# Optimization experiments

Measured on AMD Instinct MI355X. Metric: run time of the kernel, lower is better.

Reference implementation:

```python
import jax, jax.numpy as jnp
import numpy as np

TOPK = 10
NC = 80
ALPHA = 1.0
BETA = 6.0
EPS = 1e-8
IOU_EPS = 1e-7


def setup_inputs() -> dict:
    key = jax.random.key(0)
    ks = jax.random.split(key, 7)
    B, M, C = 32, 40, NC
    img = 640
    pts = []
    for s in (8, 16, 32):
        n = img // s
        xs = (jnp.arange(n, dtype=jnp.float32) + 0.5) * s
        gy, gx = jnp.meshgrid(xs, xs, indexing="ij")
        pts.append(jnp.stack([gx.ravel(), gy.ravel()], axis=-1))
    anchor_points = jnp.concatenate(pts, axis=0)  # (8400, 2)
    A = anchor_points.shape[0]
    pred_scores = jax.random.uniform(ks[0], (B, A, C), dtype=jnp.float32)
    ctr = anchor_points[None] + jax.random.normal(ks[1], (B, A, 2), dtype=jnp.float32) * 8.0
    wh = jax.random.uniform(ks[2], (B, A, 2), minval=16.0, maxval=128.0, dtype=jnp.float32)
    pred_boxes = jnp.concatenate([ctr - wh / 2, ctr + wh / 2], axis=-1)
    gctr = jax.random.uniform(ks[3], (B, M, 2), minval=64.0, maxval=576.0, dtype=jnp.float32)
    gwh = jax.random.uniform(ks[4], (B, M, 2), minval=32.0, maxval=256.0, dtype=jnp.float32)
    gt_boxes = jnp.concatenate([gctr - gwh / 2, gctr + gwh / 2], axis=-1)
    gt_labels = jax.random.randint(ks[5], (B, M, 1), 0, C)
    gt_mask = jax.random.uniform(ks[6], (B, M, 1)) < 0.8
    return {
        "pred_scores": pred_scores,
        "pred_boxes": pred_boxes,
        "anchor_points": anchor_points,
        "gt_labels": gt_labels,
        "gt_boxes": gt_boxes,
        "gt_mask": gt_mask,
    }


def reference(pred_scores, pred_boxes, anchor_points, gt_labels, gt_boxes, gt_mask):
    B, A, C = pred_scores.shape
    M = gt_boxes.shape[1]
    dt = pred_scores.dtype
    gtm = gt_mask[..., 0].astype(dt)  # (B, M)
    cls = gt_labels[..., 0].astype(jnp.int32)  # (B, M)
    b_idx = jnp.arange(B)[:, None]

    # --- step 1: anchor centers inside GT boxes ---
    lt = gt_boxes[:, :, None, :2]  # (B, M, 1, 2)
    rb = gt_boxes[:, :, None, 2:]
    ap = anchor_points[None, None, :, :]  # (1, 1, A, 2)
    deltas = jnp.concatenate([ap - lt, rb - ap], axis=-1)  # (B, M, A, 4)
    in_gt = (jnp.min(deltas, axis=-1) > EPS).astype(dt)  # (B, M, A)
    valid = in_gt * gtm[:, :, None]

    # --- alignment metric: cls score gathered per GT label, IoU(gt, pred) ---
    scores = pred_scores[b_idx, :, cls] * valid  # (B, M, A)
    gt = gt_boxes[:, :, None, :]  # (B, M, 1, 4)
    pd = pred_boxes[:, None, :, :]  # (B, 1, A, 4)
    iw = jnp.clip(jnp.minimum(gt[..., 2], pd[..., 2]) - jnp.maximum(gt[..., 0], pd[..., 0]), 0.0)
    ih = jnp.clip(jnp.minimum(gt[..., 3], pd[..., 3]) - jnp.maximum(gt[..., 1], pd[..., 1]), 0.0)
    inter = iw * ih
    area_g = (gt[..., 2] - gt[..., 0]) * (gt[..., 3] - gt[..., 1])
    area_p = (pd[..., 2] - pd[..., 0]) * (pd[..., 3] - pd[..., 1])
    ious = jnp.clip(inter / (area_g + area_p - inter + IOU_EPS), 0.0) * valid  # (B, M, A)
    align = (scores ** ALPHA) * (ious ** BETA)

    # --- step 2: top-k candidates per GT with duplicate suppression ---
    _, topk_idxs = jax.lax.top_k(align, TOPK)  # (B, M, K)
    km = jnp.broadcast_to(gt_mask[..., 0][:, :, None], topk_idxs.shape)
    topk_idxs = jnp.where(km, topk_idxs, 0)
    counts = jnp.zeros((B, M, A), dtype=jnp.int32)
    counts = counts.at[b_idx[:, :, None], jnp.arange(M)[None, :, None], topk_idxs].add(1)
    counts = jnp.where(counts > 1, 0, counts)
    mask = counts.astype(dt) * in_gt * gtm[:, :, None]  # (B, M, A)

    # --- step 4: resolve anchors assigned to multiple GTs by highest IoU ---
    fg = mask.sum(axis=1)  # (B, A)
    max_iou_onehot = jax.nn.one_hot(jnp.argmax(ious, axis=1), M, axis=1, dtype=dt)
    mask = jnp.where(fg[:, None, :] > 1, max_iou_onehot, mask)
    fg = mask.sum(axis=1)
    tgt_idx = jnp.argmax(mask, axis=1)  # (B, A)

    # --- targets ---
    target_labels = jnp.clip(jnp.take_along_axis(cls, tgt_idx, axis=1), 0, NC)  # (B, A)
    target_boxes = jnp.take_along_axis(gt_boxes, tgt_idx[..., None], axis=1)  # (B, A, 4)
    target_scores = jax.nn.one_hot(target_labels, NC, dtype=dt)
    target_scores = jnp.where(fg[..., None] > 0, target_scores, 0.0)

    # --- normalize scores by aligned metric ---
    align = align * mask
    pos_align = jnp.max(align, axis=-1, keepdims=True)  # (B, M, 1)
    pos_iou = jnp.max(ious * mask, axis=-1, keepdims=True)
    norm = jnp.max(align * pos_iou / (pos_align + EPS), axis=-2)[..., None]  # (B, A, 1)
    target_scores = target_scores * norm
    return target_labels, target_boxes, target_scores, fg > 0
```

## Files before the change

kernel.cpp:

```cpp
#include <hip/hip_runtime.h>
#include <cstdint>

#define TOPK_K 10
#define NCLS   80
#define EPS_F     1e-8f
#define IOU_EPS_F 1e-7f

__global__ void k_prep(const unsigned char* __restrict__ gm, int n,
                       int* __restrict__ gmask)
{
    __shared__ int anynz;
    if (threadIdx.x == 0) anynz = 0;
    __syncthreads();
    for (int i = threadIdx.x; i < n; i += blockDim.x) {
        if ((i & 3) && gm[i]) anynz = 1;
    }
    __syncthreads();
    const int is_int32 = (anynz == 0);
    const int* gi = (const int*)gm;
    for (int i = threadIdx.x; i < n; i += blockDim.x) {
        gmask[i] = is_int32 ? (gi[i] != 0) : (gm[i] != 0);
    }
}

__global__ __launch_bounds__(256) void k_topk(
    const float*  __restrict__ ps,
    const float4* __restrict__ pb,
    const float2* __restrict__ apts,
    const int*    __restrict__ gl,
    const float4* __restrict__ gb,
    const int*    __restrict__ gmask,
    unsigned long long* __restrict__ mask_bits,
    int B, int A, int C, int M)
{
    const int bm = blockIdx.x;
    if (!gmask[bm]) return;
    const int b = bm / M;
    const int m = bm - b * M;

    const float4 g = gb[bm];
    const float gx0 = g.x, gy0 = g.y, gx1 = g.z, gy1 = g.w;
    const float areag = (gx1 - gx0) * (gy1 - gy0);
    const int cls = gl[bm];
    const float*  psb = ps + (size_t)b * A * C + cls;
    const float4* pbb = pb + (size_t)b * A;

    float tv[TOPK_K]; int ti[TOPK_K];
#pragma unroll
    for (int i = 0; i < TOPK_K; ++i) { tv[i] = -1.0f; ti[i] = 0x7fffffff; }

    for (int a = threadIdx.x; a < A; a += blockDim.x) {
        const float2 an = apts[a];
        const float d = fminf(fminf(an.x - gx0, an.y - gy0),
                              fminf(gx1 - an.x, gy1 - an.y));
        float al = 0.0f;
        if (d > EPS_F) {
            const float4 p = pbb[a];
            const float iw = fmaxf(fminf(gx1, p.z) - fmaxf(gx0, p.x), 0.0f);
            const float ih = fmaxf(fminf(gy1, p.w) - fmaxf(gy0, p.y), 0.0f);
            const float inter = iw * ih;
            const float areap = (p.z - p.x) * (p.w - p.y);
            const float iou = fmaxf(inter / (areag + areap - inter + IOU_EPS_F), 0.0f);
            const float sc = psb[(size_t)a * C];
            const float i2 = iou * iou;
            al = sc * (i2 * i2 * i2);
        }
        if ((al > tv[TOPK_K - 1]) ||
            (al == tv[TOPK_K - 1] && a < ti[TOPK_K - 1])) {
            float cv = al; int ci = a;
#pragma unroll
            for (int q = 0; q < TOPK_K; ++q) {
                const bool bet = (cv > tv[q]) || (cv == tv[q] && ci < ti[q]);
                if (bet) {
                    const float tv_ = tv[q]; const int ti_ = ti[q];
                    tv[q] = cv; ti[q] = ci; cv = tv_; ci = ti_;
                }
            }
        }
    }

    __shared__ float sv[256];
    __shared__ int   si[256];
    const unsigned long long bit = 1ull << m;
    int p = 0;
    for (int r = 0; r < TOPK_K; ++r) {
        sv[threadIdx.x] = (p < TOPK_K) ? tv[p] : -1.0f;
        si[threadIdx.x] = (p < TOPK_K) ? ti[p] : 0x7fffffff;
        const int myci = si[threadIdx.x];
        __syncthreads();
        for (int s = 128; s > 0; s >>= 1) {
            if (threadIdx.x < s) {
                const float ov = sv[threadIdx.x + s];
                const int   oi = si[threadIdx.x + s];
                if ((ov > sv[threadIdx.x]) ||
                    (ov == sv[threadIdx.x] && oi < si[threadIdx.x])) {
                    sv[threadIdx.x] = ov; si[threadIdx.x] = oi;
                }
            }
            __syncthreads();
        }
        const int widx = si[0];
        if (threadIdx.x == 0 && widx != 0x7fffffff) {
            const float2 an = apts[widx];
            const float d = fminf(fminf(an.x - gx0, an.y - gy0),
                                  fminf(gx1 - an.x, gy1 - an.y));
            if (d > EPS_F)
                atomicOr(&mask_bits[(size_t)b * A + widx], bit);
        }
        if (myci == widx) ++p;
        __syncthreads();
    }
}

__global__ __launch_bounds__(256) void k_resolve(
    const float*  __restrict__ ps,
    const float4* __restrict__ pb,
    const float2* __restrict__ apts,
    const int*    __restrict__ gl,
    const float4* __restrict__ gb,
    const int*    __restrict__ gmask,
    const unsigned long long* __restrict__ mask_bits,
    int*          __restrict__ assign,
    float*        __restrict__ aval,
    unsigned int* __restrict__ pos_align,
    unsigned int* __restrict__ pos_iou,
    float*        __restrict__ out,
    int B, int A, int C, int M)
{
    const int id = blockIdx.x * blockDim.x + threadIdx.x;
    if (id >= B * A) return;
    const int b = id / A;
    const int a = id - b * A;

    const unsigned long long bits = mask_bits[id];
    const int cnt = __popcll(bits);
    int t = 0, fg = 0;
    const float2 an = apts[a];
    const float4 p  = pb[id];
    const float areap = (p.z - p.x) * (p.w - p.y);

    if (cnt == 1) {
        t = __ffsll(bits) - 1; fg = 1;
    } else if (cnt > 1) {
        float best = -1.0f; int bi = 0;
        for (int mm = 0; mm < M; ++mm) {
            const float4 gg = gb[b * M + mm];
            const float d = fminf(fminf(an.x - gg.x, an.y - gg.y),
                                  fminf(gg.z - an.x, gg.w - an.y));
            float iou = 0.0f;
            if (d > EPS_F && gmask[b * M + mm]) {
                const float iw = fmaxf(fminf(gg.z, p.z) - fmaxf(gg.x, p.x), 0.0f);
                const float ih = fmaxf(fminf(gg.w, p.w) - fmaxf(gg.y, p.y), 0.0f);
                const float inter = iw * ih;
                const float areag = (gg.z - gg.x) * (gg.w - gg.y);
                iou = fmaxf(inter / (areag + areap - inter + IOU_EPS_F), 0.0f);
            }
            if (iou > best) { best = iou; bi = mm; }
        }
        t = bi; fg = 1;
    }

    float av = 0.0f;
    if (fg) {
        const float4 gg = gb[b * M + t];
        const float d = fminf(fminf(an.x - gg.x, an.y - gg.y),
                              fminf(gg.z - an.x, gg.w - an.y));
        if (d > EPS_F && gmask[b * M + t]) {
            const float iw = fmaxf(fminf(gg.z, p.z) - fmaxf(gg.x, p.x), 0.0f);
            const float ih = fmaxf(fminf(gg.w, p.w) - fmaxf(gg.y, p.y), 0.0f);
            const float inter = iw * ih;
            const float areag = (gg.z - gg.x) * (gg.w - gg.y);
            const float iou = fmaxf(inter / (areag + areap - inter + IOU_EPS_F), 0.0f);
            const float sc = ps[((size_t)b * A + a) * C + gl[b * M + t]];
            const float i2 = iou * iou;
            av = sc * (i2 * i2 * i2);
            atomicMax(&pos_align[b * M + t], __float_as_uint(av));
            atomicMax(&pos_iou[b * M + t],  __float_as_uint(iou));
        }
    }

    assign[id] = t;
    aval[id]   = av;

    int lab = gl[b * M + t];
    lab = lab < 0 ? 0 : (lab > NCLS ? NCLS : lab);
    out[id] = (float)lab;
    ((float4*)(out + (size_t)B * A))[id] = gb[b * M + t];
    out[(size_t)B * A * (5 + C) + id] = fg ? 1.0f : 0.0f;
}

__global__ void k_norm(const int* __restrict__ assign,
                       const float* __restrict__ aval,
                       const unsigned int* __restrict__ pos_align,
                       const unsigned int* __restrict__ pos_iou,
                       float* __restrict__ normv, int BA, int A, int M)
{
    const int id = blockIdx.x * blockDim.x + threadIdx.x;
    if (id >= BA) return;
    const int b = id / A;
    const int t = assign[id];
    const float pa = __uint_as_float(pos_align[b * M + t]);
    const float pi = __uint_as_float(pos_iou[b * M + t]);
    normv[id] = aval[id] * pi / (pa + EPS_F);
}

__global__ void k_scores(const float* __restrict__ labels,
                         const float* __restrict__ normv,
                         float4* __restrict__ scores, int BA, int C4)
{
    const int gid = blockIdx.x * blockDim.x + threadIdx.x;
    if (gid >= BA * C4) return;
    const int row = gid / C4;
    const int c4  = gid - row * C4;
    const int lab = (int)labels[row];
    const float nv = normv[row];
    const int cb = c4 * 4;
    float4 v;
    v.x = (cb + 0 == lab) ? nv : 0.0f;
    v.y = (cb + 1 == lab) ? nv : 0.0f;
    v.z = (cb + 2 == lab) ? nv : 0.0f;
    v.w = (cb + 3 == lab) ? nv : 0.0f;
    scores[gid] = v;
}

extern "C" void kernel_launch(void* const* d_in, const int* in_sizes, int n_in,
                              void* d_out, int out_size, void* d_ws, size_t ws_size,
                              hipStream_t stream)
{
    const float*  ps = (const float*)d_in[0];
    const float4* pb = (const float4*)d_in[1];
    const float2* ap = (const float2*)d_in[2];
    const int*    gl = (const int*)d_in[3];
    const float4* gb = (const float4*)d_in[4];
    const unsigned char* gm = (const unsigned char*)d_in[5];

    const int A = in_sizes[2] / 2;
    const int B = in_sizes[1] / (A * 4);
    const int M = in_sizes[4] / (B * 4);
    const int C = in_sizes[0] / (B * A);
    const int BA = B * A;

    size_t off = 0;
    auto alloc = [&](size_t bytes) {
        void* p = (char*)d_ws + off;
        off += (bytes + 255) & ~(size_t)255;
        return p;
    };
    unsigned long long* mask_bits = (unsigned long long*)alloc((size_t)BA * 8);
    unsigned int* pos_a = (unsigned int*)alloc((size_t)B * M * 4);
    unsigned int* pos_i = (unsigned int*)alloc((size_t)B * M * 4);
    const size_t zero_bytes = off;
    int*   gmask  = (int*)alloc((size_t)B * M * 4);
    int*   assign = (int*)alloc((size_t)BA * 4);
    float* aval   = (float*)alloc((size_t)BA * 4);
    float* normv  = (float*)alloc((size_t)BA * 4);

    hipMemsetAsync(d_ws, 0, zero_bytes, stream);

    k_prep<<<1, 256, 0, stream>>>(gm, B * M, gmask);

    k_topk<<<B * M, 256, 0, stream>>>(ps, pb, ap, gl, gb, gmask, mask_bits,
                                      B, A, C, M);

    float* out = (float*)d_out;
    k_resolve<<<(BA + 255) / 256, 256, 0, stream>>>(
        ps, pb, ap, gl, gb, gmask, mask_bits,
        assign, aval, pos_a, pos_i, out, B, A, C, M);

    k_norm<<<(BA + 255) / 256, 256, 0, stream>>>(assign, aval, pos_a, pos_i,
                                                 normv, BA, A, M);

    const int C4 = C / 4;
    const int tot = BA * C4;
    k_scores<<<(tot + 255) / 256, 256, 0, stream>>>(
        out, normv, (float4*)(out + (size_t)BA * 5), BA, C4);
}
```

Baseline: 234.7 us.

## Precompute alignment matrix via coalesced score tiles, then top-k over dense rows

Adds a k_align kernel that loads 64-anchor tiles of the full score rows into shared memory with coalesced float4 reads. It computes the alignment metric for all GTs of a batch and stores it as a dense (B,M,A) buffer. This replaces the strided per-GT gathers of one class column in the old top-k kernel. Top-k now scans contiguous float4 rows using packed 64-bit keys and a wavefront shuffle reduction instead of a shared-memory tree. The memset and norm kernels are folded into the prep and score kernels, and a fallback path is kept for when the workspace is too small to hold the extra buffer.

```diff
diff --git a/kernel.cpp b/kernel.cpp
--- a/kernel.cpp
+++ b/kernel.cpp
@@ -5,9 +5,14 @@
 #define NCLS   80
 #define EPS_F     1e-8f
 #define IOU_EPS_F 1e-7f
+#define CH 64
+
+typedef unsigned long long u64;
 
 __global__ void k_prep(const unsigned char* __restrict__ gm, int n,
-                       int* __restrict__ gmask)
+                       int* __restrict__ gmask,
+                       unsigned int* __restrict__ pos_a,
+                       unsigned int* __restrict__ pos_i)
 {
     __shared__ int anynz;
     if (threadIdx.x == 0) anynz = 0;
@@ -20,106 +25,167 @@
     const int* gi = (const int*)gm;
     for (int i = threadIdx.x; i < n; i += blockDim.x) {
         gmask[i] = is_int32 ? (gi[i] != 0) : (gm[i] != 0);
-    }
-}
-
-__global__ __launch_bounds__(256) void k_topk(
+        pos_a[i] = 0u;
+        pos_i[i] = 0u;
+    }
+}
+
+__global__ __launch_bounds__(256) void k_align(
     const float*  __restrict__ ps,
     const float4* __restrict__ pb,
     const float2* __restrict__ apts,
     const int*    __restrict__ gl,
     const float4* __restrict__ gb,
     const int*    __restrict__ gmask,
-    unsigned long long* __restrict__ mask_bits,
-    int B, int A, int C, int M)
+    float*        __restrict__ align,
+    u64*          __restrict__ mask_bits,
+    int B, int A, int C, int M, int NCH)
+{
+    const int blk = blockIdx.x;
+    const int b  = blk / NCH;
+    const int ch = blk - b * NCH;
+    const int a0 = ch * CH;
+    const int aN = min(CH, A - a0);
+    const int tid = threadIdx.x;
+
+    __shared__ float  ssc[CH][81];
+    __shared__ float4 sgb[64];
+    __shared__ int    scls[64];
+    __shared__ int    sgm[64];
+
+    if (tid < aN) mask_bits[(size_t)b * A + a0 + tid] = 0ull;
+    if (tid < M) {
+        sgb[tid]  = gb[b * M + tid];
+        scls[tid] = gl[b * M + tid];
+        sgm[tid]  = gmask[b * M + tid];
+    }
+
+    const int C4 = C >> 2;
+    const float4* psrow = (const float4*)(ps + ((size_t)b * A + a0) * C);
+    for (int idx = tid; idx < aN * C4; idx += 256) {
+        const int r  = idx / C4;
+        const int c4 = idx - r * C4;
+        const float4 v = psrow[(size_t)r * C4 + c4];
+        float* dst = &ssc[r][c4 * 4];
+        dst[0] = v.x; dst[1] = v.y; dst[2] = v.z; dst[3] = v.w;
+    }
+    __syncthreads();
+
+    const int asub = tid & (CH - 1);
+    const int m0   = tid >> 6;
+    const bool act = (asub < aN);
+    float2 an = make_float2(0.f, 0.f);
+    float4 p  = make_float4(0.f, 0.f, 0.f, 0.f);
+    float areap = 0.f;
+    if (act) {
+        an = apts[a0 + asub];
+        p  = pb[(size_t)b * A + a0 + asub];
+        areap = (p.z - p.x) * (p.w - p.y);
+    }
+    for (int m = m0; m < M; m += 4) {
+        if (!act) continue;
+        float al = 0.f;
+        if (sgm[m]) {
+            const float4 g = sgb[m];
+            const float d = fminf(fminf(an.x - g.x, an.y - g.y),
+                                  fminf(g.z - an.x, g.w - an.y));
+            if (d > EPS_F) {
+                const float iw = fmaxf(fminf(g.z, p.z) - fmaxf(g.x, p.x), 0.f);
+                const float ih = fmaxf(fminf(g.w, p.w) - fmaxf(g.y, p.y), 0.f);
+                const float inter = iw * ih;
+                const float areag = (g.z - g.x) * (g.w - g.y);
+                const float iou = fmaxf(inter / (areag + areap - inter + IOU_EPS_F), 0.f);
+                const float sc = ssc[asub][scls[m]];
+                const float i2 = iou * iou;
+                al = sc * (i2 * i2 * i2);
+            }
+        }
+        align[((size_t)b * M + m) * A + a0 + asub] = al;
+    }
+}
+
+#define INS10(val, idx)                                                     \
+    {                                                                       \
+        u64 key = ((u64)__float_as_uint(val) << 32) |                       \
+                  (unsigned)(~(unsigned)(idx));                             \
+        if (key > kk[9]) {                                                  \
+            _Pragma("unroll")                                               \
+            for (int q = 0; q < 10; ++q) {                                  \
+                if (key > kk[q]) { u64 t_ = kk[q]; kk[q] = key; key = t_; } \
+            }                                                               \
+        }                                                                   \
+    }
+
+__global__ __launch_bounds__(256) void k_topk2(
+    const float4* __restrict__ align4,
+    const float2* __restrict__ apts,
+    const int*    __restrict__ gmask,
+    const float4* __restrict__ gb,
+    u64*          __restrict__ mask_bits,
+    int B, int A, int M)
 {
     const int bm = blockIdx.x;
     if (!gmask[bm]) return;
     const int b = bm / M;
     const int m = bm - b * M;
+    const int tid = threadIdx.x;
 
     const float4 g = gb[bm];
-    const float gx0 = g.x, gy0 = g.y, gx1 = g.z, gy1 = g.w;
-    const float areag = (gx1 - gx0) * (gy1 - gy0);
-    const int cls = gl[bm];
-    const float*  psb = ps + (size_t)b * A * C + cls;
-    const float4* pbb = pb + (size_t)b * A;
-
-    float tv[TOPK_K]; int ti[TOPK_K];
-#pragma unroll
-    for (int i = 0; i < TOPK_K; ++i) { tv[i] = -1.0f; ti[i] = 0x7fffffff; }
-
-    for (int a = threadIdx.x; a < A; a += blockDim.x) {
-        const float2 an = apts[a];
-        const float d = fminf(fminf(an.x - gx0, an.y - gy0),
-                              fminf(gx1 - an.x, gy1 - an.y));
-        float al = 0.0f;
-        if (d > EPS_F) {
-            const float4 p = pbb[a];
-            const float iw = fmaxf(fminf(gx1, p.z) - fmaxf(gx0, p.x), 0.0f);
-            const float ih = fmaxf(fminf(gy1, p.w) - fmaxf(gy0, p.y), 0.0f);
-            const float inter = iw * ih;
-            const float areap = (p.z - p.x) * (p.w - p.y);
-            const float iou = fmaxf(inter / (areag + areap - inter + IOU_EPS_F), 0.0f);
-            const float sc = psb[(size_t)a * C];
-            const float i2 = iou * iou;
-            al = sc * (i2 * i2 * i2);
-        }
-        if ((al > tv[TOPK_K - 1]) ||
-            (al == tv[TOPK_K - 1] && a < ti[TOPK_K - 1])) {
-            float cv = al; int ci = a;
-#pragma unroll
-            for (int q = 0; q < TOPK_K; ++q) {
-                const bool bet = (cv > tv[q]) || (cv == tv[q] && ci < ti[q]);
-                if (bet) {
-                    const float tv_ = tv[q]; const int ti_ = ti[q];
-                    tv[q] = cv; ti[q] = ci; cv = tv_; ci = ti_;
-                }
-            }
-        }
-    }
-
-    __shared__ float sv[256];
-    __shared__ int   si[256];
-    const unsigned long long bit = 1ull << m;
-    int p = 0;
+    const float4* row = align4 + (size_t)bm * (A >> 2);
+    const int n4 = A >> 2;
+
+    u64 kk[10];
+#pragma unroll
+    for (int q = 0; q < 10; ++q) kk[q] = 0ull;
+
+    for (int i = tid; i < n4; i += 256) {
+        const float4 v = row[i];
+        const int a4 = i * 4;
+        INS10(v.x, a4 + 0);
+        INS10(v.y, a4 + 1);
+        INS10(v.z, a4 + 2);
+        INS10(v.w, a4 + 3);
+    }
+
+    __shared__ u64 swv[4];
+    const u64 bit = 1ull << m;
     for (int r = 0; r < TOPK_K; ++r) {
-        sv[threadIdx.x] = (p < TOPK_K) ? tv[p] : -1.0f;
-        si[threadIdx.x] = (p < TOPK_K) ? ti[p] : 0x7fffffff;
-        const int myci = si[threadIdx.x];
+        u64 cur = kk[0];
+#pragma unroll
+        for (int off = 32; off; off >>= 1) {
+            const u64 o = __shfl_xor(cur, off);
+            cur = (o > cur) ? o : cur;
+        }
+        if ((tid & 63) == 0) swv[tid >> 6] = cur;
         __syncthreads();
-        for (int s = 128; s > 0; s >>= 1) {
-            if (threadIdx.x < s) {
-                const float ov = sv[threadIdx.x + s];
-                const int   oi = si[threadIdx.x + s];
-                if ((ov > sv[threadIdx.x]) ||
-                    (ov == sv[threadIdx.x] && oi < si[threadIdx.x])) {
-                    sv[threadIdx.x] = ov; si[threadIdx.x] = oi;
-                }
-            }
-            __syncthreads();
-        }
-        const int widx = si[0];
-        if (threadIdx.x == 0 && widx != 0x7fffffff) {
-            const float2 an = apts[widx];
-            const float d = fminf(fminf(an.x - gx0, an.y - gy0),
-                                  fminf(gx1 - an.x, gy1 - an.y));
+        const u64 w01 = (swv[0] > swv[1]) ? swv[0] : swv[1];
+        const u64 w23 = (swv[2] > swv[3]) ? swv[2] : swv[3];
+        const u64 win = (w01 > w23) ? w01 : w23;
+        if (kk[0] == win) {
+#pragma unroll
+            for (int q = 0; q < 9; ++q) kk[q] = kk[q + 1];
+            kk[9] = 0ull;
+        }
+        if (tid == 0) {
+            const unsigned a = ~(unsigned)(win & 0xFFFFFFFFull);
+            const float2 an = apts[a];
+            const float d = fminf(fminf(an.x - g.x, an.y - g.y),
+                                  fminf(g.z - an.x, g.w - an.y));
             if (d > EPS_F)
-                atomicOr(&mask_bits[(size_t)b * A + widx], bit);
-        }
-        if (myci == widx) ++p;
+                atomicOr(&mask_bits[(size_t)b * A + a], bit);
+        }
         __syncthreads();
     }
 }
 
-__global__ __launch_bounds__(256) void k_resolve(
-    const float*  __restrict__ ps,
+__global__ __launch_bounds__(256) void k_resolve2(
+    const float*  __restrict__ align,
     const float4* __restrict__ pb,
     const float2* __restrict__ apts,
     const int*    __restrict__ gl,
     const float4* __restrict__ gb,
     const int*    __restrict__ gmask,
-    const unsigned long long* __restrict__ mask_bits,
+    const u64*    __restrict__ mask_bits,
     int*          __restrict__ assign,
     float*        __restrict__ aval,
     unsigned int* __restrict__ pos_align,
@@ -132,7 +198,7 @@
     const int b = id / A;
     const int a = id - b * A;
 
-    const unsigned long long bits = mask_bits[id];
+    const u64 bits = mask_bits[id];
     const int cnt = __popcll(bits);
     int t = 0, fg = 0;
     const float2 an = apts[a];
@@ -162,6 +228,171 @@
 
     float av = 0.0f;
     if (fg) {
+        av = align[((size_t)b * M + t) * A + a];
+        const float4 gg = gb[b * M + t];
+        const float d = fminf(fminf(an.x - gg.x, an.y - gg.y),
+                              fminf(gg.z - an.x, gg.w - an.y));
+        if (d > EPS_F && gmask[b * M + t]) {
+            const float iw = fmaxf(fminf(gg.z, p.z) - fmaxf(gg.x, p.x), 0.0f);
+            const float ih = fmaxf(fminf(gg.w, p.w) - fmaxf(gg.y, p.y), 0.0f);
+            const float inter = iw * ih;
+            const float areag = (gg.z - gg.x) * (gg.w - gg.y);
+            const float iou = fmaxf(inter / (areag + areap - inter + IOU_EPS_F), 0.0f);
+            if (av  > 0.0f) atomicMax(&pos_align[b * M + t], __float_as_uint(av));
+            if (iou > 0.0f) atomicMax(&pos_iou[b * M + t],  __float_as_uint(iou));
+        }
+    }
+
+    assign[id] = t;
+    aval[id]   = av;
+
+    int lab = gl[b * M + t];
+    lab = lab < 0 ? 0 : (lab > NCLS ? NCLS : lab);
+    out[id] = (float)lab;
+    ((float4*)(out + (size_t)B * A))[id] = gb[b * M + t];
+    out[(size_t)B * A * (5 + C) + id] = fg ? 1.0f : 0.0f;
+}
+
+__global__ void k_scores2(const int* __restrict__ assign,
+                          const float* __restrict__ aval,
+                          const unsigned int* __restrict__ pos_align,
+                          const unsigned int* __restrict__ pos_iou,
+                          const int* __restrict__ gl,
+                          float4* __restrict__ scores,
+                          int BA, int A, int M, int C4)
+{
+    const int gid = blockIdx.x * blockDim.x + threadIdx.x;
+    if (gid >= BA * C4) return;
+    const int row = gid / C4;
+    const int c4  = gid - row * C4;
+    const int b   = row / A;
+    const int t   = assign[row];
+    const float av = aval[row];
+    const float pa = __uint_as_float(pos_align[b * M + t]);
+    const float pi = __uint_as_float(pos_iou[b * M + t]);
+    const float nv = av * pi / (pa + EPS_F);
+    int lab = gl[b * M + t];
+    lab = lab < 0 ? 0 : (lab > NCLS ? NCLS : lab);
+    const int cb = c4 * 4;
+    float4 v;
+    v.x = (cb + 0 == lab) ? nv : 0.0f;
+    v.y = (cb + 1 == lab) ? nv : 0.0f;
+    v.z = (cb + 2 == lab) ? nv : 0.0f;
+    v.w = (cb + 3 == lab) ? nv : 0.0f;
+    scores[gid] = v;
+}
+
+__global__ __launch_bounds__(256) void k_topk_fb(
+    const float*  __restrict__ ps, const float4* __restrict__ pb,
+    const float2* __restrict__ apts, const int* __restrict__ gl,
+    const float4* __restrict__ gb, const int* __restrict__ gmask,
+    u64* __restrict__ mask_bits, int B, int A, int C, int M)
+{
+    const int bm = blockIdx.x;
+    if (!gmask[bm]) return;
+    const int b = bm / M;
+    const int m = bm - b * M;
+    const float4 g = gb[bm];
+    const float areag = (g.z - g.x) * (g.w - g.y);
+    const int cls = gl[bm];
+    const float*  psb = ps + (size_t)b * A * C + cls;
+    const float4* pbb = pb + (size_t)b * A;
+    const int tid = threadIdx.x;
+
+    u64 kk[10];
+#pragma unroll
+    for (int q = 0; q < 10; ++q) kk[q] = 0ull;
+
+    for (int a = tid; a < A; a += 256) {
+        const float2 an = apts[a];
+        const float d = fminf(fminf(an.x - g.x, an.y - g.y),
+                              fminf(g.z - an.x, g.w - an.y));
+        float al = 0.0f;
+        if (d > EPS_F) {
+            const float4 p = pbb[a];
+            const float iw = fmaxf(fminf(g.z, p.z) - fmaxf(g.x, p.x), 0.0f);
+            const float ih = fmaxf(fminf(g.w, p.w) - fmaxf(g.y, p.y), 0.0f);
+            const float inter = iw * ih;
+            const float areap = (p.z - p.x) * (p.w - p.y);
+            const float iou = fmaxf(inter / (areag + areap - inter + IOU_EPS_F), 0.0f);
+            const float sc = psb[(size_t)a * C];
+            const float i2 = iou * iou;
+            al = sc * (i2 * i2 * i2);
+        }
+        INS10(al, a);
+    }
+
+    __shared__ u64 swv[4];
+    const u64 bit = 1ull << m;
+    for (int r = 0; r < TOPK_K; ++r) {
+        u64 cur = kk[0];
+#pragma unroll
+        for (int off = 32; off; off >>= 1) {
+            const u64 o = __shfl_xor(cur, off);
+            cur = (o > cur) ? o : cur;
+        }
+        if ((tid & 63) == 0) swv[tid >> 6] = cur;
+        __syncthreads();
+        const u64 w01 = (swv[0] > swv[1]) ? swv[0] : swv[1];
+        const u64 w23 = (swv[2] > swv[3]) ? swv[2] : swv[3];
+        const u64 win = (w01 > w23) ? w01 : w23;
+        if (kk[0] == win) {
+#pragma unroll
+            for (int q = 0; q < 9; ++q) kk[q] = kk[q + 1];
+            kk[9] = 0ull;
+        }
+        if (tid == 0) {
+            const unsigned a = ~(unsigned)(win & 0xFFFFFFFFull);
+            const float2 an = apts[a];
+            const float d = fminf(fminf(an.x - g.x, an.y - g.y),
+                                  fminf(g.z - an.x, g.w - an.y));
+            if (d > EPS_F)
+                atomicOr(&mask_bits[(size_t)b * A + a], bit);
+        }
+        __syncthreads();
+    }
+}
+
+__global__ __launch_bounds__(256) void k_resolve_fb(
+    const float*  __restrict__ ps, const float4* __restrict__ pb,
+    const float2* __restrict__ apts, const int* __restrict__ gl,
+    const float4* __restrict__ gb, const int* __restrict__ gmask,
+    const u64* __restrict__ mask_bits,
+    int* __restrict__ assign, float* __restrict__ aval,
+    unsigned int* __restrict__ pos_align, unsigned int* __restrict__ pos_iou,
+    float* __restrict__ out, int B, int A, int C, int M)
+{
+    const int id = blockIdx.x * blockDim.x + threadIdx.x;
+    if (id >= B * A) return;
+    const int b = id / A;
+    const int a = id - b * A;
+    const u64 bits = mask_bits[id];
+    const int cnt = __popcll(bits);
+    int t = 0, fg = 0;
+    const float2 an = apts[a];
+    const float4 p  = pb[id];
+    const float areap = (p.z - p.x) * (p.w - p.y);
+    if (cnt == 1) { t = __ffsll(bits) - 1; fg = 1; }
+    else if (cnt > 1) {
+        float best = -1.0f; int bi = 0;
+        for (int mm = 0; mm < M; ++mm) {
+            const float4 gg = gb[b * M + mm];
+            const float d = fminf(fminf(an.x - gg.x, an.y - gg.y),
+                                  fminf(gg.z - an.x, gg.w - an.y));
+            float iou = 0.0f;
+            if (d > EPS_F && gmask[b * M + mm]) {
+                const float iw = fmaxf(fminf(gg.z, p.z) - fmaxf(gg.x, p.x), 0.0f);
+                const float ih = fmaxf(fminf(gg.w, p.w) - fmaxf(gg.y, p.y), 0.0f);
+                const float inter = iw * ih;
+                const float areag = (gg.z - gg.x) * (gg.w - gg.y);
+                iou = fmaxf(inter / (areag + areap - inter + IOU_EPS_F), 0.0f);
+            }
+            if (iou > best) { best = iou; bi = mm; }
+        }
+        t = bi; fg = 1;
+    }
+    float av = 0.0f;
+    if (fg) {
         const float4 gg = gb[b * M + t];
         const float d = fminf(fminf(an.x - gg.x, an.y - gg.y),
                               fminf(gg.z - an.x, gg.w - an.y));
@@ -174,14 +405,12 @@
             const float sc = ps[((size_t)b * A + a) * C + gl[b * M + t]];
             const float i2 = iou * iou;
             av = sc * (i2 * i2 * i2);
-            atomicMax(&pos_align[b * M + t], __float_as_uint(av));
-            atomicMax(&pos_iou[b * M + t],  __float_as_uint(iou));
-        }
-    }
-
+            if (av  > 0.0f) atomicMax(&pos_align[b * M + t], __float_as_uint(av));
+            if (iou > 0.0f) atomicMax(&pos_iou[b * M + t],  __float_as_uint(iou));
+        }
+    }
     assign[id] = t;
     aval[id]   = av;
-
     int lab = gl[b * M + t];
     lab = lab < 0 ? 0 : (lab > NCLS ? NCLS : lab);
     out[id] = (float)lab;
@@ -189,38 +418,10 @@
     out[(size_t)B * A * (5 + C) + id] = fg ? 1.0f : 0.0f;
 }
 
-__global__ void k_norm(const int* __restrict__ assign,
-                       const float* __restrict__ aval,
-                       const unsigned int* __restrict__ pos_align,
-                       const unsigned int* __restrict__ pos_iou,
-                       float* __restrict__ normv, int BA, int A, int M)
+__global__ void k_zero64(u64* __restrict__ p, int n)
 {
     const int id = blockIdx.x * blockDim.x + threadIdx.x;
-    if (id >= BA) return;
-    const int b = id / A;
-    const int t = assign[id];
-    const float pa = __uint_as_float(pos_align[b * M + t]);
-    const float pi = __uint_as_float(pos_iou[b * M + t]);
-    normv[id] = aval[id] * pi / (pa + EPS_F);
-}
-
-__global__ void k_scores(const float* __restrict__ labels,
-                         const float* __restrict__ normv,
-                         float4* __restrict__ scores, int BA, int C4)
-{
-    const int gid = blockIdx.x * blockDim.x + threadIdx.x;
-    if (gid >= BA * C4) return;
-    const int row = gid / C4;
-    const int c4  = gid - row * C4;
-    const int lab = (int)labels[row];
-    const float nv = normv[row];
-    const int cb = c4 * 4;
-    float4 v;
-    v.x = (cb + 0 == lab) ? nv : 0.0f;
-    v.y = (cb + 1 == lab) ? nv : 0.0f;
-    v.z = (cb + 2 == lab) ? nv : 0.0f;
-    v.w = (cb + 3 == lab) ? nv : 0.0f;
-    scores[gid] = v;
+    if (id < n) p[id] = 0ull;
 }
 
 extern "C" void kernel_launch(void* const* d_in, const int* in_sizes, int n_in,
@@ -239,6 +440,7 @@
     const int M = in_sizes[4] / (B * 4);
     const int C = in_sizes[0] / (B * A);
     const int BA = B * A;
+    const int C4 = C / 4;
 
     size_t off = 0;
     auto alloc = [&](size_t bytes) {
@@ -246,32 +448,39 @@
         off += (bytes + 255) & ~(size_t)255;
         return p;
     };
-    unsigned long long* mask_bits = (unsigned long long*)alloc((size_t)BA * 8);
+    u64*   mask_bits = (u64*)alloc((size_t)BA * 8);
     unsigned int* pos_a = (unsigned int*)alloc((size_t)B * M * 4);
     unsigned int* pos_i = (unsigned int*)alloc((size_t)B * M * 4);
-    const size_t zero_bytes = off;
     int*   gmask  = (int*)alloc((size_t)B * M * 4);
     int*   assign = (int*)alloc((size_t)BA * 4);
     float* aval   = (float*)alloc((size_t)BA * 4);
-    float* normv  = (float*)alloc((size_t)BA * 4);
-
-    hipMemsetAsync(d_ws, 0, zero_bytes, stream);
-
-    k_prep<<<1, 256, 0, stream>>>(gm, B * M, gmask);
-
-    k_topk<<<B * M, 256, 0, stream>>>(ps, pb, ap, gl, gb, gmask, mask_bits,
-                                      B, A, C, M);
+    float* align  = (float*)alloc((size_t)BA * M * 4);
+    const bool big_ws = (off <= ws_size);
 
     float* out = (float*)d_out;
-    k_resolve<<<(BA + 255) / 256, 256, 0, stream>>>(
-        ps, pb, ap, gl, gb, gmask, mask_bits,
-        assign, aval, pos_a, pos_i, out, B, A, C, M);
-
-    k_norm<<<(BA + 255) / 256, 256, 0, stream>>>(assign, aval, pos_a, pos_i,
-                                                 normv, BA, A, M);
-
-    const int C4 = C / 4;
+
+    k_prep<<<1, 256, 0, stream>>>(gm, B * M, gmask, pos_a, pos_i);
+
+    if (big_ws) {
+        const int NCH = (A + CH - 1) / CH;
+        k_align<<<B * NCH, 256, 0, stream>>>(ps, pb, ap, gl, gb, gmask,
+                                             align, mask_bits, B, A, C, M, NCH);
+        k_topk2<<<B * M, 256, 0, stream>>>((const float4*)align, ap, gmask, gb,
+                                           mask_bits, B, A, M);
+        k_resolve2<<<(BA + 255) / 256, 256, 0, stream>>>(
+            align, pb, ap, gl, gb, gmask, mask_bits,
+            assign, aval, pos_a, pos_i, out, B, A, C, M);
+    } else {
+        k_zero64<<<(BA + 255) / 256, 256, 0, stream>>>(mask_bits, BA);
+        k_topk_fb<<<B * M, 256, 0, stream>>>(ps, pb, ap, gl, gb, gmask,
+                                             mask_bits, B, A, C, M);
+        k_resolve_fb<<<(BA + 255) / 256, 256, 0, stream>>>(
+            ps, pb, ap, gl, gb, gmask, mask_bits,
+            assign, aval, pos_a, pos_i, out, B, A, C, M);
+    }
+
     const int tot = BA * C4;
-    k_scores<<<(tot + 255) / 256, 256, 0, stream>>>(
-        out, normv, (float4*)(out + (size_t)BA * 5), BA, C4);
-}
+    k_scores2<<<(tot + 255) / 256, 256, 0, stream>>>(
+        assign, aval, pos_a, pos_i, gl,
+        (float4*)(out + (size_t)BA * 5), BA, A, M, C4);
+}
```

After: 242.7 us. 1.03x slower.
